# Kernel tuning notes

Measured on AMD Instinct MI355X. Metric: run time of the kernel, lower is better.

Reference implementation:

```python
import jax, jax.numpy as jnp
import numpy as np
from jax import lax

B = 2; C = 256; NH = 8; NP = 4; NUM_LAYERS = 6; FFN = 1024
IN_SIZES = (512, 1024, 2048)
LVL_SHAPES = ((64, 64), (32, 32), (16, 16), (8, 8), (4, 4))
NL = len(LVL_SHAPES); DH = C // NH
N = sum(h * w for h, w in LVL_SHAPES)  # 5456 tokens over the pyramid


def _ln(x, g, b):
    m = x.mean(-1, keepdims=True)
    v = x.var(-1, keepdims=True)
    return (x - m) * lax.rsqrt(v + 1e-5) * g + b


def _gn(x, g, b, groups=8):
    Bb, Cc, Hh, Ww = x.shape
    xr = x.reshape(Bb, groups, Cc // groups, Hh, Ww)
    m = xr.mean((2, 3, 4), keepdims=True)
    v = xr.var((2, 3, 4), keepdims=True)
    xr = (xr - m) * lax.rsqrt(v + 1e-5)
    return xr.reshape(Bb, Cc, Hh, Ww) * g[None, :, None, None] + b[None, :, None, None]


def _conv(x, w, b, stride, pad):
    y = lax.conv_general_dilated(x, w, (stride, stride), [(pad, pad), (pad, pad)],
                                 dimension_numbers=('NCHW', 'OIHW', 'NCHW'))
    return y + b[None, :, None, None]


def _priors():
    # normalized (cx, cy) anchor centers per pyramid location
    pr = []
    for (fh, fw) in LVL_SHAPES:
        cy = (jnp.arange(fh, dtype=jnp.float32) + 0.5) / fh
        cx = (jnp.arange(fw, dtype=jnp.float32) + 0.5) / fw
        gy, gx = jnp.meshgrid(cy, cx, indexing='ij')
        pr.append(jnp.stack([gx, gy], -1).reshape(-1, 2))
    return jnp.concatenate(pr, 0)  # [N,2]


def _sample(vl, loc, fh, fw):
    # vl: [B,NH,S_l,DH] flattened level values; loc: [B,N,NH,NP,2] in [0,1]
    x = loc[..., 0] * fw - 0.5
    y = loc[..., 1] * fh - 0.5
    x0 = jnp.floor(x); y0 = jnp.floor(y)
    lx = x - x0; ly = y - y0

    def gather(xi, yi):
        inb = ((xi >= 0) & (xi <= fw - 1) & (yi >= 0) & (yi <= fh - 1)).astype(vl.dtype)
        xc = jnp.clip(xi, 0, fw - 1).astype(jnp.int32)
        yc = jnp.clip(yi, 0, fh - 1).astype(jnp.int32)
        idx = (yc * fw + xc).transpose(0, 2, 1, 3).reshape(B, NH, N * NP)
        g = jnp.take_along_axis(vl, idx[..., None], axis=2)  # [B,NH,N*NP,DH]
        g = g.reshape(B, NH, N, NP, DH).transpose(0, 2, 1, 3, 4)  # [B,N,NH,NP,DH]
        return g * inb[..., None]

    return (gather(x0, y0) * ((1 - lx) * (1 - ly))[..., None]
            + gather(x0 + 1, y0) * (lx * (1 - ly))[..., None]
            + gather(x0, y0 + 1) * ((1 - lx) * ly)[..., None]
            + gather(x0 + 1, y0 + 1) * (lx * ly)[..., None])


def _attn_layer(x, priors, g1, b1_, woff, boff, watt, batt, wval, bval, wout, bout):
    q = _ln(x, g1, b1_)
    off = (q @ woff + boff).reshape(B, N, NH, NL, NP, 2)
    att = jax.nn.softmax((q @ watt + batt).reshape(B, N, NH, NL * NP), axis=-1)
    att = att.reshape(B, N, NH, NL, NP)
    val = (q @ wval + bval).reshape(B, N, NH, DH)
    normz = jnp.array([[w, h] for (h, w) in LVL_SHAPES], jnp.float32)  # (W,H) per level
    loc = priors[None, :, None, None, None, :] + off / normz[None, None, None, :, None, :]
    out = jnp.zeros((B, N, NH, DH), x.dtype)
    start = 0
    for l, (fh, fw) in enumerate(LVL_SHAPES):
        vl = val[:, start:start + fh * fw].transpose(0, 2, 1, 3)  # [B,NH,S_l,DH]
        s = _sample(vl, loc[:, :, :, l], fh, fw)  # [B,N,NH,NP,DH]
        out = out + (s * att[:, :, :, l, :, None]).sum(3)
        start += fh * fw
    return x + out.reshape(B, N, C) @ wout + bout


def _ffn(x, g2, b2_, w1, b1_, w2, b2_2):
    h = jax.nn.relu(_ln(x, g2, b2_) @ w1 + b1_)
    return x + h @ w2 + b2_2


def _forward(in_map0, in_map1, in_map2, pw0, pb0, pw1, pb1, pw2, pb2,
             buw0, bub0, gng, gnb, buw1, bub1,
             ln1g, ln1b, woff, boff, watt, batt, wval, bval, wout, bout,
             ln2g, ln2b, w1, b1, w2, b2):
    maps = [_conv(in_map0, pw0, pb0, 1, 0), _conv(in_map1, pw1, pb1, 1, 0), _conv(in_map2, pw2, pb2, 1, 0)]
    m = _conv(in_map2, buw0, bub0, 2, 1)  # bottom-up from raw C5 (2048ch)
    maps.append(m)
    m = _conv(jax.nn.relu(_gn(m, gng, gnb)), buw1, bub1, 2, 1)
    maps.append(m)
    feats = jnp.concatenate([mm.reshape(B, C, -1).transpose(0, 2, 1) for mm in maps], axis=1)  # [B,N,C]
    priors = _priors()
    for i in range(NUM_LAYERS):
        feats = _attn_layer(feats, priors, ln1g[i], ln1b[i], woff[i], boff[i],
                            watt[i], batt[i], wval[i], bval[i], wout[i], bout[i])
        feats = _ffn(feats, ln2g[i], ln2b[i], w1[i], b1[i], w2[i], b2[i])
    return feats


def setup_inputs():
    key = jax.random.key(0)
    ks = list(jax.random.split(key, 40)); ki = iter(ks)
    def rn(shape, s=0.02):
        return jax.random.normal(next(ki), shape, jnp.float32) * s
    inp = {}
    for i, (cs, (h, w)) in enumerate(zip(IN_SIZES, LVL_SHAPES[:3])):
        inp[f"in_map{i}"] = jax.random.normal(next(ki), (B, cs, h, w), jnp.float32)
    for i, cs in enumerate(IN_SIZES):
        inp[f"pw{i}"] = rn((C, cs, 1, 1)); inp[f"pb{i}"] = jnp.zeros((C,), jnp.float32)
    inp["buw0"] = rn((C, IN_SIZES[-1], 3, 3)); inp["bub0"] = jnp.zeros((C,), jnp.float32)
    inp["gng"] = jnp.ones((C,), jnp.float32); inp["gnb"] = jnp.zeros((C,), jnp.float32)
    inp["buw1"] = rn((C, C, 3, 3)); inp["bub1"] = jnp.zeros((C,), jnp.float32)
    LYR = NUM_LAYERS
    inp["ln1g"] = jnp.ones((LYR, C), jnp.float32); inp["ln1b"] = jnp.zeros((LYR, C), jnp.float32)
    inp["woff"] = rn((LYR, C, NH * NL * NP * 2), 0.01)
    th = np.arange(NH) * (2.0 * np.pi / NH)
    grid = np.stack([np.cos(th), np.sin(th)], -1)
    grid = grid / np.abs(grid).max(-1, keepdims=True)  # [NH,2]
    boff = np.tile(grid[:, None, None, :], (1, NL, NP, 1)) * (np.arange(NP) + 1)[None, None, :, None]
    inp["boff"] = jnp.tile(jnp.asarray(boff.reshape(-1), jnp.float32)[None], (LYR, 1))
    inp["watt"] = rn((LYR, C, NH * NL * NP), 0.01); inp["batt"] = jnp.zeros((LYR, NH * NL * NP), jnp.float32)
    inp["wval"] = rn((LYR, C, C)); inp["bval"] = jnp.zeros((LYR, C), jnp.float32)
    inp["wout"] = rn((LYR, C, C)); inp["bout"] = jnp.zeros((LYR, C), jnp.float32)
    inp["ln2g"] = jnp.ones((LYR, C), jnp.float32); inp["ln2b"] = jnp.zeros((LYR, C), jnp.float32)
    inp["w1"] = rn((LYR, C, FFN)); inp["b1"] = jnp.zeros((LYR, FFN), jnp.float32)
    inp["w2"] = rn((LYR, FFN, C)); inp["b2"] = jnp.zeros((LYR, C), jnp.float32)
    return inp


def reference(in_map0, in_map1, in_map2, pw0, pb0, pw1, pb1, pw2, pb2,
              buw0, bub0, gng, gnb, buw1, bub1,
              ln1g, ln1b, woff, boff, watt, batt, wval, bval, wout, bout,
              ln2g, ln2b, w1, b1, w2, b2):
    feats = _forward(in_map0, in_map1, in_map2, pw0, pb0, pw1, pb1, pw2, pb2,
                     buw0, bub0, gng, gnb, buw1, bub1,
                     ln1g, ln1b, woff, boff, watt, batt, wval, bval, wout, bout,
                     ln2g, ln2b, w1, b1, w2, b2)
    outs = []
    start = 0
    for (fh, fw) in LVL_SHAPES:
        outs.append(feats[:, start:start + fh * fw].transpose(0, 2, 1).reshape(B, C, fh, fw))
        start += fh * fw
    return tuple(outs)
```

## Files before the change

### kernel.cpp

```cpp
#include <hip/hip_runtime.h>
#include <cstdint>

typedef long long i64;
typedef unsigned short u16;
typedef __attribute__((ext_vector_type(8))) short short8;
typedef __attribute__((ext_vector_type(8))) unsigned short us8;
typedef __attribute__((ext_vector_type(4))) float f32x4;

#define NTOK 5456
#define BNROWS 10912
#define NLAYERS 6

__device__ __forceinline__ u16 f2bf(float f) {
  unsigned u = __float_as_uint(f);
  return (u16)((u + 0x7FFFu + ((u >> 16) & 1u)) >> 16);
}
__device__ __forceinline__ float bf2f(u16 h) {
  return __uint_as_float(((unsigned)h) << 16);
}

template<int BNT>
__global__ __launch_bounds__(256) void mgemm_k(
    const u16* __restrict__ A, const u16* __restrict__ B, int K,
    float* __restrict__ C, float* __restrict__ C2, u16* __restrict__ C16, i64 sCm,
    const float* __restrict__ bias, int relu, int addres, int qkv,
    int M, int N, int mbsh, i64 bCz,
    int KS, float* __restrict__ part)
{
  constexpr int NW = BNT / 32;
  __shared__ u16 Asm[2][128 * 64];
  __shared__ u16 Bsm[2][BNT * 64];
  int tid = threadIdx.x;

  int bx = blockIdx.x, by = blockIdx.y;
  int gx = gridDim.x, gy = gridDim.y;
  int nwg = gx * gy;
  if (KS == 1 && nwg >= 16) {
    int lin = bx + gx * by;
    int xcd = lin & 7, k = lin >> 3;
    int q = nwg >> 3, r = nwg & 7;
    int f = (xcd < r) ? (xcd * (q + 1) + k) : (r * (q + 1) + (xcd - r) * q + k);
    bx = f / gy;
    by = f - bx * gy;
  }
  int m0 = bx * 128, n0 = by * BNT;

  int ks = blockIdx.z;
  int Kc = K / KS;
  int k0 = ks * Kc;
  int lane = tid & 63, w = tid >> 6;
  int wr = w >> 1, wc = w & 1;
  int r16 = lane & 15, g = lane >> 4;

  f32x4 acc[4][NW];
#pragma unroll
  for (int mi = 0; mi < 4; mi++)
#pragma unroll
    for (int nj = 0; nj < NW; nj++) acc[mi][nj] = (f32x4){0.f, 0.f, 0.f, 0.f};

  const u16* Ag = A + (i64)m0 * K + k0;
  const u16* Bg = B + (i64)n0 * K + k0;
  int nt = Kc >> 6;

  auto stage = [&](int buf, int kt) {
#pragma unroll
    for (int r = 0; r < 4; r++) {
      int s = r * 256 + tid;
      int row = s >> 3, c = s & 7;
      int cs = ((c ^ (row & 7)) << 3);
      __builtin_amdgcn_global_load_lds(
          (const __attribute__((address_space(1))) void*)(Ag + (i64)row * K + kt + cs),
          (__attribute__((address_space(3))) void*)(&Asm[buf][(r * 256 + (w << 6)) << 3]),
          16, 0, 0);
    }
#pragma unroll
    for (int r = 0; r < NW; r++) {
      int s = r * 256 + tid;
      int row = s >> 3, c = s & 7;
      int cs = ((c ^ (row & 7)) << 3);
      __builtin_amdgcn_global_load_lds(
          (const __attribute__((address_space(1))) void*)(Bg + (i64)row * K + kt + cs),
          (__attribute__((address_space(3))) void*)(&Bsm[buf][(r * 256 + (w << 6)) << 3]),
          16, 0, 0);
    }
  };

  stage(0, 0);
  __syncthreads();
  for (int t = 0; t < nt; t++) {
    int cur = t & 1;
    if (t + 1 < nt) stage(cur ^ 1, (t + 1) << 6);
#pragma unroll
    for (int h = 0; h < 2; h++) {
      short8 av[4], bv[NW];
#pragma unroll
      for (int mi = 0; mi < 4; mi++) {
        int row = wr * 64 + mi * 16 + r16;
        av[mi] = *(const short8*)&Asm[cur][row * 64 + ((((h << 2) + g) ^ (row & 7)) << 3)];
      }
#pragma unroll
      for (int nj = 0; nj < NW; nj++) {
        int row = wc * (NW * 16) + nj * 16 + r16;
        bv[nj] = *(const short8*)&Bsm[cur][row * 64 + ((((h << 2) + g) ^ (row & 7)) << 3)];
      }
#pragma unroll
      for (int mi = 0; mi < 4; mi++)
#pragma unroll
        for (int nj = 0; nj < NW; nj++)
          acc[mi][nj] = __builtin_amdgcn_mfma_f32_16x16x32_bf16(
              av[mi], bv[nj], acc[mi][nj], 0, 0, 0);
    }
    __syncthreads();
  }

  if (KS > 1) {
#pragma unroll
    for (int mi = 0; mi < 4; mi++)
#pragma unroll
      for (int nj = 0; nj < NW; nj++)
#pragma unroll
        for (int r = 0; r < 4; r++) {
          int grow = m0 + wr * 64 + mi * 16 + g * 4 + r;
          int gcol = n0 + wc * (NW * 16) + nj * 16 + r16;
          if (grow < M) part[((i64)ks * M + grow) * N + gcol] = acc[mi][nj][r];
        }
  } else if (qkv) {
    u16* off16 = (u16*)C;
    u16* att16 = (u16*)C2;
#pragma unroll
    for (int mi = 0; mi < 4; mi++)
#pragma unroll
      for (int nj = 0; nj < NW; nj++)
#pragma unroll
        for (int r = 0; r < 4; r++) {
          int grow = m0 + wr * 64 + mi * 16 + g * 4 + r;
          int gcol = n0 + wc * (NW * 16) + nj * 16 + r16;
          if (grow < M) {
            float v = acc[mi][nj][r] + bias[gcol];
            if (gcol < 320) off16[(i64)grow * 320 + gcol] = f2bf(v);
            else if (gcol < 480) att16[(i64)grow * 160 + (gcol - 320)] = f2bf(v);
            else if (gcol < 736) C16[(i64)grow * 256 + (gcol - 480)] = f2bf(v);
          }
        }
  } else {
    float bv[NW];
    int gc0 = n0 + wc * (NW * 16) + r16;
#pragma unroll
    for (int nj = 0; nj < NW; nj++)
      bv[nj] = bias ? bias[gc0 + nj * 16] : 0.f;
    int mask = (1 << mbsh) - 1;
#pragma unroll
    for (int mi = 0; mi < 4; mi++) {
#pragma unroll
      for (int r = 0; r < 4; r++) {
        int grow = m0 + wr * 64 + mi * 16 + g * 4 + r;
        if (grow >= M) continue;
        i64 rowb = (i64)(grow >> mbsh) * bCz + (i64)(grow & mask) * sCm;
#pragma unroll
        for (int nj = 0; nj < NW; nj++) {
          int gcol = gc0 + nj * 16;
          if (gcol >= N) continue;
          float v = acc[mi][nj][r] + bv[nj];
          if (relu) v = fmaxf(v, 0.f);
          i64 ci = rowb + gcol;
          if (C16) C16[ci] = f2bf(v);
          else {
            if (addres) v += C[ci];
            C[ci] = v;
          }
        }
      }
    }
  }
}

__global__ __launch_bounds__(256, 1) void ffn_fused_k(
    const u16* __restrict__ qb, const u16* __restrict__ w1n,
    const u16* __restrict__ w2n, const float* __restrict__ b1,
    const float* __restrict__ b2, float* __restrict__ feats, int M)
{
  __shared__ u16 B1s[2][64 * 256];
  __shared__ u16 B2s[2][256 * 64];
  __shared__ u16 Hs[64 * 88];
  __shared__ float b1s[1024];
  int tid = threadIdx.x;
  int lane = tid & 63, w = tid >> 6;
  int wr = w >> 1, wc = w & 1;
  int r16 = lane & 15, g = lane >> 4;
  int m0 = blockIdx.x * 64;

  for (int i = tid; i < 1024; i += 256) b1s[i] = b1[i];

  short8 av_all[8][2];
#pragma unroll
  for (int ks = 0; ks < 8; ks++)
#pragma unroll
    for (int mi = 0; mi < 2; mi++) {
      int row = m0 + wr * 32 + mi * 16 + r16;
      av_all[ks][mi] = *(const short8*)(qb + (i64)row * 256 + ks * 32 + g * 8);
    }

  auto stageW = [&](int buf, int ch) {
#pragma unroll
    for (int r = 0; r < 8; r++) {
      int s = r * 256 + tid;
      int row = s >> 5, c = s & 31;
      int cs = ((c ^ (row & 7)) << 3);
      __builtin_amdgcn_global_load_lds(
          (const __attribute__((address_space(1))) void*)(w1n + (i64)(ch * 64 + row) * 256 + cs),
          (__attribute__((address_space(3))) void*)(&B1s[buf][(r * 256 + (w << 6)) << 3]),
          16, 0, 0);
    }
#pragma unroll
    for (int r = 0; r < 8; r++) {
      int s = r * 256 + tid;
      int row = s >> 3, c = s & 7;
      int cs = ((c ^ (row & 7)) << 3);
      __builtin_amdgcn_global_load_lds(
          (const __attribute__((address_space(1))) void*)(w2n + (i64)row * 1024 + ch * 64 + cs),
          (__attribute__((address_space(3))) void*)(&B2s[buf][(r * 256 + (w << 6)) << 3]),
          16, 0, 0);
    }
  };

  f32x4 acc2[2][8];
#pragma unroll
  for (int mi = 0; mi < 2; mi++)
#pragma unroll
    for (int nj = 0; nj < 8; nj++) acc2[mi][nj] = (f32x4){0.f, 0.f, 0.f, 0.f};

  stageW(0, 0);
  __syncthreads();

  int cur = 0;
  for (int ch = 0; ch < 16; ch++) {
    if (ch + 1 < 16) stageW(cur ^ 1, ch + 1);

    f32x4 acc1[2][2];
#pragma unroll
    for (int mi = 0; mi < 2; mi++)
#pragma unroll
      for (int nj = 0; nj < 2; nj++) acc1[mi][nj] = (f32x4){0.f, 0.f, 0.f, 0.f};
#pragma unroll
    for (int ks = 0; ks < 8; ks++) {
      short8 bv[2];
#pragma unroll
      for (int nj = 0; nj < 2; nj++) {
        int row = wc * 32 + nj * 16 + r16;
        bv[nj] = *(const short8*)&B1s[cur][row * 256 + ((((ks << 2) + g) ^ (row & 7)) << 3)];
      }
#pragma unroll
      for (int mi = 0; mi < 2; mi++)
#pragma unroll
        for (int nj = 0; nj < 2; nj++)
          acc1[mi][nj] = __builtin_amdgcn_mfma_f32_16x16x32_bf16(
              av_all[ks][mi], bv[nj], acc1[mi][nj], 0, 0, 0);
    }
#pragma unroll
    for (int mi = 0; mi < 2; mi++)
#pragma unroll
      for (int nj = 0; nj < 2; nj++)
#pragma unroll
        for (int r = 0; r < 4; r++) {
          int row_h = wr * 32 + mi * 16 + g * 4 + r;
          int col_h = wc * 32 + nj * 16 + r16;
          float v = acc1[mi][nj][r] + b1s[ch * 64 + col_h];
          Hs[row_h * 88 + col_h] = f2bf(fmaxf(v, 0.f));
        }
    __syncthreads();

#pragma unroll
    for (int hh = 0; hh < 2; hh++) {
      short8 av2[2], bv2[8];
#pragma unroll
      for (int mi = 0; mi < 2; mi++) {
        int row = wr * 32 + mi * 16 + r16;
        av2[mi] = *(const short8*)&Hs[row * 88 + ((hh << 2) + g) * 8];
      }
#pragma unroll
      for (int nj = 0; nj < 8; nj++) {
        int n = wc * 128 + nj * 16 + r16;
        bv2[nj] = *(const short8*)&B2s[cur][n * 64 + ((((hh << 2) + g) ^ (n & 7)) << 3)];
      }
#pragma unroll
      for (int mi = 0; mi < 2; mi++)
#pragma unroll
        for (int nj = 0; nj < 8; nj++)
          acc2[mi][nj] = __builtin_amdgcn_mfma_f32_16x16x32_bf16(
              av2[mi], bv2[nj], acc2[mi][nj], 0, 0, 0);
    }
    __syncthreads();
    cur ^= 1;
  }

#pragma unroll
  for (int mi = 0; mi < 2; mi++)
#pragma unroll
    for (int r = 0; r < 4; r++) {
      int grow = m0 + wr * 32 + mi * 16 + g * 4 + r;
      if (grow >= M) continue;
#pragma unroll
      for (int nj = 0; nj < 8; nj++) {
        int col = wc * 128 + nj * 16 + r16;
        i64 ci = (i64)grow * 256 + col;
        feats[ci] += acc2[mi][nj][r] + b2[col];
      }
    }
}

__global__ void reduce_k(const float* __restrict__ part, float* __restrict__ C,
    const float* __restrict__ bias, int mbsh, i64 bCz, i64 sCm, int M, int N, int KS)
{
  int idx = blockIdx.x * 256 + threadIdx.x;
  if (idx >= M * N) return;
  int m = idx / N, n = idx - m * N;
  float v = bias ? bias[n] : 0.f;
  for (int ks = 0; ks < KS; ks++) v += part[((i64)ks * M + m) * N + n];
  C[(i64)(m >> mbsh) * bCz + (i64)(m & ((1 << mbsh) - 1)) * sCm + n] = v;
}

__global__ void cvt_w_pro_k(const float* __restrict__ pw0, const float* __restrict__ pw1,
    const float* __restrict__ pw2, const float* __restrict__ buw0,
    const float* __restrict__ buw1, u16* __restrict__ dst)
{
  int idx = blockIdx.x * 256 + threadIdx.x;
  if (idx >= 6225920) return;
  float v;
  if (idx < 131072) v = pw0[idx];
  else if (idx < 393216) v = pw1[idx - 131072];
  else if (idx < 917504) v = pw2[idx - 393216];
  else if (idx < 5636096) v = buw0[idx - 917504];
  else v = buw1[idx - 5636096];
  dst[idx] = f2bf(v);
}

__global__ void cvt_w_layer_k(const float* __restrict__ woff, const float* __restrict__ watt,
    const float* __restrict__ wval, const float* __restrict__ wout,
    const float* __restrict__ w1, const float* __restrict__ w2, u16* __restrict__ dst)
{
  int L = blockIdx.y;
  int o = blockIdx.x * 256 + threadIdx.x;
  if (o >= 786432) return;
  u16* d = dst + (i64)L * 786432;
  float v;
  if (o < 196608) {
    int n = o >> 8, k = o & 255;
    if (n < 320) v = woff[(i64)L * 81920 + k * 320 + n];
    else if (n < 480) v = watt[(i64)L * 40960 + k * 160 + (n - 320)];
    else if (n < 736) v = wval[(i64)L * 65536 + k * 256 + (n - 480)];
    else v = 0.f;
  } else if (o < 262144) {
    int o2 = o - 196608; int n = o2 >> 8, k = o2 & 255;
    v = wout[(i64)L * 65536 + k * 256 + n];
  } else if (o < 524288) {
    int o2 = o - 262144; int n = o2 >> 8, k = o2 & 255;
    v = w1[(i64)L * 262144 + (i64)k * 1024 + n];
  } else {
    int o2 = o - 524288; int n = o2 >> 10, k = o2 & 1023;
    v = w2[(i64)L * 262144 + (i64)k * 256 + n];
  }
  d[o] = f2bf(v);
}

__global__ void cvt_bias_k(const float* __restrict__ boff, const float* __restrict__ batt,
    const float* __restrict__ bval, float* __restrict__ bq)
{
  int idx = blockIdx.x * 256 + threadIdx.x;
  if (idx >= NLAYERS * 768) return;
  int L = idx / 768, n = idx - L * 768;
  float v;
  if (n < 320) v = boff[(i64)L * 320 + n];
  else if (n < 480) v = batt[(i64)L * 160 + (n - 320)];
  else if (n < 736) v = bval[(i64)L * 256 + (n - 480)];
  else v = 0.f;
  bq[idx] = v;
}

__global__ void cvt_a_proj_k(const float* __restrict__ in, u16* __restrict__ out,
                             int P, int K)
{
  i64 o = (i64)blockIdx.x * 256 + threadIdx.x;
  if (o >= (i64)2 * P * K) return;
  int m = (int)(o / K), k = (int)(o % K);
  int b = m / P, p = m - b * P;
  out[o] = f2bf(in[((i64)b * K + k) * P + p]);
}

__global__ void im2col_bf16_k(const float* __restrict__ in, u16* __restrict__ out,
    int Cin, int Hin, int Win, int Ho, int Wo)
{
  int Kk = Cin * 9;
  i64 total = (i64)2 * Ho * Wo * Kk;
  i64 o = (i64)blockIdx.x * 256 + threadIdx.x;
  if (o >= total) return;
  int k = (int)(o % Kk);
  int m = (int)(o / Kk);
  int hw = Ho * Wo;
  int b = m / hw, pix = m - b * hw;
  int oy = pix / Wo, ox = pix - oy * Wo;
  int ci = k / 9, r = k - ci * 9;
  int ky = r / 3, kx = r - ky * 3;
  int iy = oy * 2 - 1 + ky, ix = ox * 2 - 1 + kx;
  float v = 0.f;
  if (iy >= 0 && iy < Hin && ix >= 0 && ix < Win)
    v = in[(((i64)b * Cin + ci) * Hin + iy) * Win + ix];
  out[o] = f2bf(v);
}

__global__ void gn_relu_k(const float* __restrict__ feats, float* __restrict__ y,
    const float* __restrict__ g, const float* __restrict__ bt)
{
  int grp = blockIdx.x, b = blockIdx.y;
  int tid = threadIdx.x;
  const float* fb = feats + ((i64)b * NTOK + 5376) * 256 + grp * 32;
  float s = 0.f, ss = 0.f;
  for (int i = tid; i < 2048; i += 256) {
    int cl = i >> 6, p = i & 63;
    float v = fb[(i64)p * 256 + cl];
    s += v; ss += v * v;
  }
  __shared__ float sb[4], ssb[4];
#pragma unroll
  for (int o = 32; o > 0; o >>= 1) { s += __shfl_down(s, o); ss += __shfl_down(ss, o); }
  int wv = tid >> 6;
  if ((tid & 63) == 0) { sb[wv] = s; ssb[wv] = ss; }
  __syncthreads();
  float ts = sb[0] + sb[1] + sb[2] + sb[3];
  float tss = ssb[0] + ssb[1] + ssb[2] + ssb[3];
  float mean = ts * (1.f / 2048.f);
  float rs = rsqrtf(tss * (1.f / 2048.f) - mean * mean + 1e-5f);
  for (int i = tid; i < 2048; i += 256) {
    int cl = i >> 6, p = i & 63;
    int c = grp * 32 + cl;
    float v = (fb[(i64)p * 256 + cl] - mean) * rs * g[c] + bt[c];
    y[((i64)b * 256 + c) * 64 + p] = fmaxf(v, 0.f);
  }
}

__global__ __launch_bounds__(256) void ln_k(const float* __restrict__ x,
    u16* __restrict__ y, const float* __restrict__ g, const float* __restrict__ bt,
    int rows)
{
  int row = blockIdx.x * 4 + (threadIdx.x >> 6);
  if (row >= rows) return;
  int lane = threadIdx.x & 63;
  float4 v = ((const float4*)(x + (i64)row * 256))[lane];
  float s = v.x + v.y + v.z + v.w;
  float ss = v.x * v.x + v.y * v.y + v.z * v.z + v.w * v.w;
#pragma unroll
  for (int o = 32; o > 0; o >>= 1) { s += __shfl_down(s, o); ss += __shfl_down(ss, o); }
  s = __shfl(s, 0);
  ss = __shfl(ss, 0);
  float mean = s * (1.f / 256.f);
  float rs = rsqrtf(ss * (1.f / 256.f) - mean * mean + 1e-5f);
  float4 gg = ((const float4*)g)[lane];
  float4 bb = ((const float4*)bt)[lane];
  ushort4 o4;
  o4.x = f2bf((v.x - mean) * rs * gg.x + bb.x);
  o4.y = f2bf((v.y - mean) * rs * gg.y + bb.y);
  o4.z = f2bf((v.z - mean) * rs * gg.z + bb.z);
  o4.w = f2bf((v.w - mean) * rs * gg.w + bb.w);
  ((ushort4*)(y + (i64)row * 256))[lane] = o4;
}

__global__ __launch_bounds__(256) void dsample_k(
    const u16* __restrict__ val, const u16* __restrict__ off,
    const u16* __restrict__ att, u16* __restrict__ out)
{
  const int FH[5] = {64, 32, 16, 8, 4};
  const int ST[5] = {0, 4096, 5120, 5376, 5440};
  int bid = blockIdx.x;
  int chunk = (bid & 7) * 86 + (bid >> 3);
  if (chunk >= 682) return;
  int lane = threadIdx.x & 63;
  int half = lane >> 5;
  int l32 = lane & 31;
  int t = chunk * 8 + ((threadIdx.x >> 6) << 1) + half;
  int b = blockIdx.y;
  int h = l32 >> 2, d4 = l32 & 3;

  int lv;
  if (t < 4096)      lv = 0;
  else if (t < 5120) lv = 1;
  else if (t < 5376) lv = 2;
  else if (t < 5440) lv = 3;
  else               lv = 4;
  int loc = t - ST[lv];
  int sh = 6 - lv;
  int py = loc >> sh, px = loc - (py << sh);
  float inv = 1.f / (float)FH[lv];
  float prx = (px + 0.5f) * inv, pry = (py + 0.5f) * inv;
  i64 bt = (i64)b * NTOK + t;
  const u16* offp = off + bt * 320 + h * 40;
  const u16* attp = att + bt * 160 + h * 20;
  const u16* vbase = val + ((i64)b * NTOK) * 256 + h * 32 + d4 * 8;

  float own_a[5], own_fx[5], own_fy[5];
  int own_pk[5];
  float mx = -1e30f;
#pragma unroll
  for (int j = 0; j < 5; j++) {
    float lg = bf2f(attp[d4 + 4 * j]);
    own_a[j] = lg;
    mx = fmaxf(mx, lg);
  }
  mx = fmaxf(mx, __shfl_xor(mx, 1));
  mx = fmaxf(mx, __shfl_xor(mx, 2));
  float sum = 0.f;
#pragma unroll
  for (int j = 0; j < 5; j++) {
    float e = __expf(own_a[j] - mx);
    own_a[j] = e;
    sum += e;
  }
  sum += __shfl_xor(sum, 1);
  sum += __shfl_xor(sum, 2);
  float rinv = 1.f / sum;
#pragma unroll
  for (int j = 0; j < 5; j++) {
    int p = d4 + 4 * j;
    own_a[j] *= rinv;
    unsigned opk = *(const unsigned*)(offp + 2 * p);
    float ox = bf2f((u16)(opk & 0xFFFF));
    float oy = bf2f((u16)(opk >> 16));
    float sff = (float)(64 >> j);
    float xx = prx * sff + ox - 0.5f;
    float yy = pry * sff + oy - 0.5f;
    float xf = floorf(xx), yf = floorf(yy);
    own_fx[j] = xx - xf;
    own_fy[j] = yy - yf;
    own_pk[j] = (((int)yf) << 16) | (((int)xf) & 0xFFFF);
  }

  float acc[8] = {0.f, 0.f, 0.f, 0.f, 0.f, 0.f, 0.f, 0.f};
#pragma unroll
  for (int p = 0; p < 20; p++) {
    const int j = p >> 2;
    const int sf = FH[j], st = ST[j];
    int src = (half << 5) | (h << 2) | (p & 3);
    float wa = __shfl(own_a[j], src);
    float fx = __shfl(own_fx[j], src);
    float fy = __shfl(own_fy[j], src);
    int pk = __shfl(own_pk[j], src);
    int x0 = (pk << 16) >> 16;
    int y0 = pk >> 16;
    float gx0 = wa - wa * fx, gx1 = wa * fx;
    float w00 = gx0 - gx0 * fy, w01 = gx0 * fy;
    float w10 = gx1 - gx1 * fy, w11 = gx1 * fy;
    bool xin0 = (x0 >= 0) & (x0 < sf), xin1 = (x0 + 1 >= 0) & (x0 + 1 < sf);
    bool yin0 = (y0 >= 0) & (y0 < sf), yin1 = (y0 + 1 >= 0) & (y0 + 1 < sf);
    int ibase = st + y0 * sf + x0;
#define FMA8(W, IDX) { \
      us8 v = *(const us8*)(vbase + (i64)(IDX) * 256); \
      acc[0] = fmaf(W, bf2f(v[0]), acc[0]); acc[1] = fmaf(W, bf2f(v[1]), acc[1]); \
      acc[2] = fmaf(W, bf2f(v[2]), acc[2]); acc[3] = fmaf(W, bf2f(v[3]), acc[3]); \
      acc[4] = fmaf(W, bf2f(v[4]), acc[4]); acc[5] = fmaf(W, bf2f(v[5]), acc[5]); \
      acc[6] = fmaf(W, bf2f(v[6]), acc[6]); acc[7] = fmaf(W, bf2f(v[7]), acc[7]); }
    if (xin0 & yin0) FMA8(w00, ibase);
    if (xin1 & yin0) FMA8(w10, ibase + 1);
    if (xin0 & yin1) FMA8(w01, ibase + sf);
    if (xin1 & yin1) FMA8(w11, ibase + sf + 1);
#undef FMA8
  }
  us8 o;
#pragma unroll
  for (int i = 0; i < 8; i++) o[i] = f2bf(acc[i]);
  *(us8*)(out + ((bt * 8 + h) * 32 + d4 * 8)) = o;
}

__global__ __launch_bounds__(256) void untranspose_all_k(
    const float* __restrict__ feats, float* __restrict__ out)
{
  int u = blockIdx.x;
  int pt0, start, S; i64 ooff;
  if (u < 128)      { pt0 = u;       start = 0;    S = 4096; ooff = 0; }
  else if (u < 160) { pt0 = u - 128; start = 4096; S = 1024; ooff = 2097152; }
  else if (u < 168) { pt0 = u - 160; start = 5120; S = 256;  ooff = 2621440; }
  else if (u < 170) { pt0 = u - 168; start = 5376; S = 64;   ooff = 2752512; }
  else              { pt0 = 0;       start = 5440; S = 16;   ooff = 2785280; }
  __shared__ float tile[32][33];
  int pt = pt0 * 32, ct = blockIdx.y * 32, b = blockIdx.z;
  int tx = threadIdx.x & 31, ty = threadIdx.x >> 5;
  for (int i = ty; i < 32; i += 8) {
    int p = pt + i;
    tile[i][tx] = (p < S) ? feats[((i64)b * NTOK + start + p) * 256 + ct + tx] : 0.f;
  }
  __syncthreads();
  for (int i = ty; i < 32; i += 8) {
    int c = ct + i, p = pt + tx;
    if (p < S) out[ooff + ((i64)b * 256 + c) * S + p] = tile[tx][i];
  }
}

extern "C" void kernel_launch(void* const* d_in, const int* in_sizes, int n_in,
                              void* d_out, int out_size, void* d_ws, size_t ws_size,
                              hipStream_t stream)
{
  const float* in0  = (const float*)d_in[0];
  const float* in1  = (const float*)d_in[1];
  const float* in2  = (const float*)d_in[2];
  const float* pw0  = (const float*)d_in[3];
  const float* pb0  = (const float*)d_in[4];
  const float* pw1  = (const float*)d_in[5];
  const float* pb1  = (const float*)d_in[6];
  const float* pw2  = (const float*)d_in[7];
  const float* pb2  = (const float*)d_in[8];
  const float* buw0 = (const float*)d_in[9];
  const float* bub0 = (const float*)d_in[10];
  const float* gng  = (const float*)d_in[11];
  const float* gnb  = (const float*)d_in[12];
  const float* buw1 = (const float*)d_in[13];
  const float* bub1 = (const float*)d_in[14];
  const float* ln1g = (const float*)d_in[15];
  const float* ln1b = (const float*)d_in[16];
  const float* woff = (const float*)d_in[17];
  const float* boff = (const float*)d_in[18];
  const float* watt = (const float*)d_in[19];
  const float* batt = (const float*)d_in[20];
  const float* wval = (const float*)d_in[21];
  const float* bval = (const float*)d_in[22];
  const float* wout = (const float*)d_in[23];
  const float* bout = (const float*)d_in[24];
  const float* ln2g = (const float*)d_in[25];
  const float* ln2b = (const float*)d_in[26];
  const float* w1   = (const float*)d_in[27];
  const float* b1   = (const float*)d_in[28];
  const float* w2   = (const float*)d_in[29];
  const float* b2   = (const float*)d_in[30];
  float* out = (float*)d_out;

  const i64 TC = (i64)NTOK * 256;

  float* ws    = (float*)d_ws;
  float* feats = ws;
  u16*   qb    = (u16*)(feats + 2793472);
  u16*   valb  = qb + 2818048;
  u16*   sampb = valb + 2818048;
  float* U     = (float*)(sampb + 2818048);
  u16*   off16 = (u16*)U;
  u16*   att16 = off16 + 3491840;
  u16*   abuf  = (u16*)U;
  float* part  = U + 2097152;
  u16*   wb    = (u16*)(U + 5637120);
  float* bqkv  = (float*)(wb + 10944512);
  float* m4gn  = bqkv + 4608;

  auto mg128 = [&](dim3 grid, const u16* A, const u16* B, int K,
                   float* C, float* C2, u16* C16, i64 sCm, const float* bias,
                   int relu, int addres, int qkv, int M, int N, int mbsh, i64 bCz, int KS) {
    mgemm_k<128><<<grid, dim3(256), 0, stream>>>(A, B, K, C, C2, C16, sCm, bias,
        relu, addres, qkv, M, N, mbsh, bCz, KS, part);
  };
  auto mg64 = [&](dim3 grid, const u16* A, const u16* B, int K,
                  float* C, u16* C16, i64 sCm, const float* bias,
                  int relu, int addres, int M, int N, int mbsh, i64 bCz, int KS) {
    mgemm_k<64><<<grid, dim3(256), 0, stream>>>(A, B, K, C, nullptr, C16, sCm, bias,
        relu, addres, 0, M, N, mbsh, bCz, KS, part);
  };

  cvt_w_pro_k<<<dim3(24320), dim3(256), 0, stream>>>(pw0, pw1, pw2, buw0, buw1, wb);
  cvt_w_layer_k<<<dim3(3072, NLAYERS), dim3(256), 0, stream>>>(
      woff, watt, wval, wout, w1, w2, wb + 6225920);
  cvt_bias_k<<<dim3(18), dim3(256), 0, stream>>>(boff, batt, bval, bqkv);

  cvt_a_proj_k<<<dim3(16384), dim3(256), 0, stream>>>(in0, abuf, 4096, 512);
  mg64(dim3(64, 4, 1), abuf, wb, 512, feats, nullptr, 256, pb0, 0, 0,
       8192, 256, 12, TC, 1);
  cvt_a_proj_k<<<dim3(8192), dim3(256), 0, stream>>>(in1, abuf, 1024, 1024);
  mg64(dim3(16, 4, 2), abuf, wb + 131072, 1024, nullptr, nullptr, 256, nullptr, 0, 0,
       2048, 256, 10, 0, 2);
  reduce_k<<<dim3(2048), dim3(256), 0, stream>>>(part, feats + (i64)4096 * 256, pb1,
      10, TC, 256, 2048, 256, 2);
  cvt_a_proj_k<<<dim3(4096), dim3(256), 0, stream>>>(in2, abuf, 256, 2048);
  mg64(dim3(4, 4, 4), abuf, wb + 393216, 2048, nullptr, nullptr, 256, nullptr, 0, 0,
       512, 256, 8, 0, 4);
  reduce_k<<<dim3(512), dim3(256), 0, stream>>>(part, feats + (i64)5120 * 256, pb2,
      8, TC, 256, 512, 256, 4);

  im2col_bf16_k<<<dim3(9216), dim3(256), 0, stream>>>(in2, abuf, 2048, 16, 16, 8, 8);
  mg64(dim3(1, 4, 16), abuf, wb + 917504, 18432, nullptr, nullptr, 256, nullptr, 0, 0,
       128, 256, 6, 0, 16);
  reduce_k<<<dim3(128), dim3(256), 0, stream>>>(part, feats + (i64)5376 * 256, bub0,
      6, TC, 256, 128, 256, 16);

  gn_relu_k<<<dim3(8, 2), dim3(256), 0, stream>>>(feats, m4gn, gng, gnb);
  im2col_bf16_k<<<dim3(288), dim3(256), 0, stream>>>(m4gn, abuf, 256, 8, 8, 4, 4);
  mg64(dim3(1, 4, 4), abuf, wb + 5636096, 2304, nullptr, nullptr, 256, nullptr, 0, 0,
       32, 256, 4, 0, 4);
  reduce_k<<<dim3(32), dim3(256), 0, stream>>>(part, feats + (i64)5440 * 256, bub1,
      4, TC, 256, 32, 256, 4);

  for (int i = 0; i < NLAYERS; i++) {
    const u16* wbL = wb + 6225920 + (i64)i * 786432;
    ln_k<<<dim3(2728), dim3(256), 0, stream>>>(feats, qb,
        ln1g + (i64)i * 256, ln1b + (i64)i * 256, BNROWS);
    mg128(dim3(86, 6, 1), qb, wbL, 256, (float*)off16, (float*)att16, valb, 0,
          bqkv + (i64)i * 768, 0, 0, 1, BNROWS, 768, 14, 0, 1);
    dsample_k<<<dim3(688, 2), dim3(256), 0, stream>>>(valb, off16, att16, sampb);
    mg64(dim3(86, 4, 1), sampb, wbL + 196608, 256, feats, nullptr, 256,
         bout + (i64)i * 256, 0, 1, BNROWS, 256, 14, 0, 1);
    ln_k<<<dim3(2728), dim3(256), 0, stream>>>(feats, qb,
        ln2g + (i64)i * 256, ln2b + (i64)i * 256, BNROWS);
    ffn_fused_k<<<dim3(171), dim3(256), 0, stream>>>(qb, wbL + 262144,
        wbL + 524288, b1 + (i64)i * 1024, b2 + (i64)i * 256, feats, BNROWS);
  }

  untranspose_all_k<<<dim3(171, 8, 2), dim3(256), 0, stream>>>(feats, out);
  (void)in_sizes; (void)n_in; (void)out_size; (void)ws_size;
}
```

Before: 1.009 ms.

## Fuse second LayerNorm into FFN kernel and use 512-thread blocks

Drops the separate LayerNorm launch before the FFN. The fused FFN kernel now reads the fp32 residual rows itself, computes mean and variance with wave shuffles, and writes normalized bf16 activations into a swizzled shared-memory tile that reuses the second weight buffer. Blocks grow to 8 waves, each owning 16 rows instead of 32, which halves per-wave MFMA work and register accumulators and aims to improve latency hiding. Variance is computed as E[x^2]-mean^2, which is slightly less numerically robust, and the last block reads residual rows past M.

```diff
diff --git a/kernel.cpp b/kernel.cpp
--- a/kernel.cpp
+++ b/kernel.cpp
@@ -174,138 +174,159 @@
   }
 }
 
-__global__ __launch_bounds__(256, 1) void ffn_fused_k(
-    const u16* __restrict__ qb, const u16* __restrict__ w1n,
+__global__ __launch_bounds__(512, 1) void ffn_fused_k(
+    float* __restrict__ feats, const u16* __restrict__ w1n,
     const u16* __restrict__ w2n, const float* __restrict__ b1,
-    const float* __restrict__ b2, float* __restrict__ feats, int M)
+    const float* __restrict__ b2, const float* __restrict__ lng,
+    const float* __restrict__ lnb, int M)
 {
   __shared__ u16 B1s[2][64 * 256];
   __shared__ u16 B2s[2][256 * 64];
   __shared__ u16 Hs[64 * 88];
   __shared__ float b1s[1024];
+  u16* As = &B1s[1][0];
+
   int tid = threadIdx.x;
   int lane = tid & 63, w = tid >> 6;
   int wr = w >> 1, wc = w & 1;
   int r16 = lane & 15, g = lane >> 4;
   int m0 = blockIdx.x * 64;
 
-  for (int i = tid; i < 1024; i += 256) b1s[i] = b1[i];
-
-  short8 av_all[8][2];
-#pragma unroll
-  for (int ks = 0; ks < 8; ks++)
-#pragma unroll
-    for (int mi = 0; mi < 2; mi++) {
-      int row = m0 + wr * 32 + mi * 16 + r16;
-      av_all[ks][mi] = *(const short8*)(qb + (i64)row * 256 + ks * 32 + g * 8);
-    }
-
   auto stageW = [&](int buf, int ch) {
 #pragma unroll
-    for (int r = 0; r < 8; r++) {
-      int s = r * 256 + tid;
+    for (int r = 0; r < 4; r++) {
+      int s = r * 512 + tid;
       int row = s >> 5, c = s & 31;
       int cs = ((c ^ (row & 7)) << 3);
       __builtin_amdgcn_global_load_lds(
           (const __attribute__((address_space(1))) void*)(w1n + (i64)(ch * 64 + row) * 256 + cs),
-          (__attribute__((address_space(3))) void*)(&B1s[buf][(r * 256 + (w << 6)) << 3]),
+          (__attribute__((address_space(3))) void*)(&B1s[buf][(r * 512 + (w << 6)) << 3]),
           16, 0, 0);
     }
 #pragma unroll
-    for (int r = 0; r < 8; r++) {
-      int s = r * 256 + tid;
+    for (int r = 0; r < 4; r++) {
+      int s = r * 512 + tid;
       int row = s >> 3, c = s & 7;
       int cs = ((c ^ (row & 7)) << 3);
       __builtin_amdgcn_global_load_lds(
           (const __attribute__((address_space(1))) void*)(w2n + (i64)row * 1024 + ch * 64 + cs),
-          (__attribute__((address_space(3))) void*)(&B2s[buf][(r * 256 + (w << 6)) << 3]),
+          (__attribute__((address_space(3))) void*)(&B2s[buf][(r * 512 + (w << 6)) << 3]),
           16, 0, 0);
     }
   };
 
-  f32x4 acc2[2][8];
-#pragma unroll
-  for (int mi = 0; mi < 2; mi++)
-#pragma unroll
-    for (int nj = 0; nj < 8; nj++) acc2[mi][nj] = (f32x4){0.f, 0.f, 0.f, 0.f};
-
   stageW(0, 0);
+  for (int i = tid; i < 1024; i += 512) b1s[i] = b1[i];
+
+  {
+    int rw = tid >> 3, c0 = (tid & 7) * 32;
+    const float* fr = feats + (i64)(m0 + rw) * 256 + c0;
+    float4 x[8];
+    float s = 0.f, ss = 0.f;
+#pragma unroll
+    for (int j = 0; j < 8; j++) {
+      x[j] = ((const float4*)fr)[j];
+      s += x[j].x + x[j].y + x[j].z + x[j].w;
+      ss += x[j].x * x[j].x + x[j].y * x[j].y + x[j].z * x[j].z + x[j].w * x[j].w;
+    }
+#pragma unroll
+    for (int o = 1; o <= 4; o <<= 1) { s += __shfl_xor(s, o); ss += __shfl_xor(ss, o); }
+    float mean = s * (1.f / 256.f);
+    float rs = rsqrtf(ss * (1.f / 256.f) - mean * mean + 1e-5f);
+    const float4* gp = (const float4*)(lng + c0);
+    const float4* bp = (const float4*)(lnb + c0);
+#pragma unroll
+    for (int j = 0; j < 8; j += 2) {
+      float4 g0 = gp[j], g1 = gp[j + 1];
+      float4 b0 = bp[j], b1_ = bp[j + 1];
+      us8 o;
+      o[0] = f2bf((x[j].x - mean) * rs * g0.x + b0.x);
+      o[1] = f2bf((x[j].y - mean) * rs * g0.y + b0.y);
+      o[2] = f2bf((x[j].z - mean) * rs * g0.z + b0.z);
+      o[3] = f2bf((x[j].w - mean) * rs * g0.w + b0.w);
+      o[4] = f2bf((x[j + 1].x - mean) * rs * g1.x + b1_.x);
+      o[5] = f2bf((x[j + 1].y - mean) * rs * g1.y + b1_.y);
+      o[6] = f2bf((x[j + 1].z - mean) * rs * g1.z + b1_.z);
+      o[7] = f2bf((x[j + 1].w - mean) * rs * g1.w + b1_.w);
+      int gr = (tid & 7) * 4 + (j >> 1);
+      *(us8*)&As[rw * 256 + ((gr ^ (rw & 7)) << 3)] = o;
+    }
+  }
   __syncthreads();
+
+  short8 av_all[8];
+  {
+    int row = wr * 16 + r16;
+#pragma unroll
+    for (int ks = 0; ks < 8; ks++)
+      av_all[ks] = *(const short8*)&As[row * 256 + (((ks * 4 + g) ^ (row & 7)) << 3)];
+  }
+  __syncthreads();
+
+  f32x4 acc2[8];
+#pragma unroll
+  for (int nj = 0; nj < 8; nj++) acc2[nj] = (f32x4){0.f, 0.f, 0.f, 0.f};
 
   int cur = 0;
   for (int ch = 0; ch < 16; ch++) {
     if (ch + 1 < 16) stageW(cur ^ 1, ch + 1);
 
-    f32x4 acc1[2][2];
-#pragma unroll
-    for (int mi = 0; mi < 2; mi++)
-#pragma unroll
-      for (int nj = 0; nj < 2; nj++) acc1[mi][nj] = (f32x4){0.f, 0.f, 0.f, 0.f};
+    f32x4 acc1[2];
+#pragma unroll
+    for (int nj = 0; nj < 2; nj++) acc1[nj] = (f32x4){0.f, 0.f, 0.f, 0.f};
 #pragma unroll
     for (int ks = 0; ks < 8; ks++) {
       short8 bv[2];
 #pragma unroll
       for (int nj = 0; nj < 2; nj++) {
         int row = wc * 32 + nj * 16 + r16;
-        bv[nj] = *(const short8*)&B1s[cur][row * 256 + ((((ks << 2) + g) ^ (row & 7)) << 3)];
+        bv[nj] = *(const short8*)&B1s[cur][row * 256 + (((ks * 4 + g) ^ (row & 7)) << 3)];
       }
 #pragma unroll
-      for (int mi = 0; mi < 2; mi++)
-#pragma unroll
-        for (int nj = 0; nj < 2; nj++)
-          acc1[mi][nj] = __builtin_amdgcn_mfma_f32_16x16x32_bf16(
-              av_all[ks][mi], bv[nj], acc1[mi][nj], 0, 0, 0);
-    }
-#pragma unroll
-    for (int mi = 0; mi < 2; mi++)
-#pragma unroll
       for (int nj = 0; nj < 2; nj++)
-#pragma unroll
-        for (int r = 0; r < 4; r++) {
-          int row_h = wr * 32 + mi * 16 + g * 4 + r;
-          int col_h = wc * 32 + nj * 16 + r16;
-          float v = acc1[mi][nj][r] + b1s[ch * 64 + col_h];
-          Hs[row_h * 88 + col_h] = f2bf(fmaxf(v, 0.f));
-        }
+        acc1[nj] = __builtin_amdgcn_mfma_f32_16x16x32_bf16(
+            av_all[ks], bv[nj], acc1[nj], 0, 0, 0);
+    }
+#pragma unroll
+    for (int nj = 0; nj < 2; nj++)
+#pragma unroll
+      for (int r = 0; r < 4; r++) {
+        int hr = wr * 16 + g * 4 + r;
+        int hc = wc * 32 + nj * 16 + r16;
+        float v = acc1[nj][r] + b1s[ch * 64 + hc];
+        Hs[hr * 88 + hc] = f2bf(fmaxf(v, 0.f));
+      }
     __syncthreads();
 
 #pragma unroll
     for (int hh = 0; hh < 2; hh++) {
-      short8 av2[2], bv2[8];
-#pragma unroll
-      for (int mi = 0; mi < 2; mi++) {
-        int row = wr * 32 + mi * 16 + r16;
-        av2[mi] = *(const short8*)&Hs[row * 88 + ((hh << 2) + g) * 8];
-      }
+      short8 av2 = *(const short8*)&Hs[(wr * 16 + r16) * 88 + hh * 32 + g * 8];
+      short8 bv2[8];
 #pragma unroll
       for (int nj = 0; nj < 8; nj++) {
         int n = wc * 128 + nj * 16 + r16;
-        bv2[nj] = *(const short8*)&B2s[cur][n * 64 + ((((hh << 2) + g) ^ (n & 7)) << 3)];
+        bv2[nj] = *(const short8*)&B2s[cur][n * 64 + (((hh * 4 + g) ^ (n & 7)) << 3)];
       }
 #pragma unroll
-      for (int mi = 0; mi < 2; mi++)
-#pragma unroll
-        for (int nj = 0; nj < 8; nj++)
-          acc2[mi][nj] = __builtin_amdgcn_mfma_f32_16x16x32_bf16(
-              av2[mi], bv2[nj], acc2[mi][nj], 0, 0, 0);
+      for (int nj = 0; nj < 8; nj++)
+        acc2[nj] = __builtin_amdgcn_mfma_f32_16x16x32_bf16(
+            av2, bv2[nj], acc2[nj], 0, 0, 0);
     }
     __syncthreads();
     cur ^= 1;
   }
 
 #pragma unroll
-  for (int mi = 0; mi < 2; mi++)
-#pragma unroll
-    for (int r = 0; r < 4; r++) {
-      int grow = m0 + wr * 32 + mi * 16 + g * 4 + r;
-      if (grow >= M) continue;
-#pragma unroll
-      for (int nj = 0; nj < 8; nj++) {
-        int col = wc * 128 + nj * 16 + r16;
-        i64 ci = (i64)grow * 256 + col;
-        feats[ci] += acc2[mi][nj][r] + b2[col];
-      }
-    }
+  for (int r = 0; r < 4; r++) {
+    int grow = m0 + wr * 16 + g * 4 + r;
+    if (grow >= M) continue;
+#pragma unroll
+    for (int nj = 0; nj < 8; nj++) {
+      int col = wc * 128 + nj * 16 + r16;
+      i64 ci = (i64)grow * 256 + col;
+      feats[ci] += acc2[nj][r] + b2[col];
+    }
+  }
 }
 
 __global__ void reduce_k(const float* __restrict__ part, float* __restrict__ C,
@@ -699,10 +720,9 @@
     dsample_k<<<dim3(688, 2), dim3(256), 0, stream>>>(valb, off16, att16, sampb);
     mg64(dim3(86, 4, 1), sampb, wbL + 196608, 256, feats, nullptr, 256,
          bout + (i64)i * 256, 0, 1, BNROWS, 256, 14, 0, 1);
-    ln_k<<<dim3(2728), dim3(256), 0, stream>>>(feats, qb,
+    ffn_fused_k<<<dim3(171), dim3(512), 0, stream>>>(feats, wbL + 262144,
+        wbL + 524288, b1 + (i64)i * 1024, b2 + (i64)i * 256,
         ln2g + (i64)i * 256, ln2b + (i64)i * 256, BNROWS);
-    ffn_fused_k<<<dim3(171), dim3(256), 0, stream>>>(qb, wbL + 262144,
-        wbL + 524288, b1 + (i64)i * 1024, b2 + (i64)i * 256, feats, BNROWS);
   }
 
   untranspose_all_k<<<dim3(171, 8, 2), dim3(256), 0, stream>>>(feats, out);
```

After: 957.4 us (median of 2 runs). 5.1% less time.
